# Kernel tuning notes

Hardware: AMD Instinct MI355X
Metric: run time of the kernel (lower is better)

Reference implementation:

```python
import jax, jax.numpy as jnp
import numpy as np

B, S, D, H, SEP = 4, 2048, 768, 8, 102
Dh = D // H


def layer_norm(x, g, b, eps=1e-5):
    m = jnp.mean(x, axis=-1, keepdims=True)
    v = jnp.var(x, axis=-1, keepdims=True)
    return (x - m) / jnp.sqrt(v + eps) * g + b


def setup_inputs() -> dict:
    key = jax.random.key(0)
    ks = jax.random.split(key, 16)
    hidden_states = jax.random.normal(ks[0], (B, S, D), dtype=jnp.float32)
    # input_ids: random vocab ids avoiding SEP, with two SEP tokens planted per row
    rng = np.random.default_rng(0)
    ids = rng.integers(103, 30000, size=(B, S))
    for b in range(B):
        ids[b, S // 3 + 7 * b] = SEP
        ids[b, 2 * S // 3 + 11 * b] = SEP
    input_ids = jnp.asarray(ids, dtype=jnp.int64)
    attention_mask = jnp.ones((B, S), dtype=jnp.int32)
    sc = 0.02
    p = {}
    p['Wq'] = jax.random.normal(ks[1], (D, D), jnp.float32) * sc
    p['bq'] = jnp.zeros((D,), jnp.float32)
    p['Wk'] = jax.random.normal(ks[2], (D, D), jnp.float32) * sc
    p['bk'] = jnp.zeros((D,), jnp.float32)
    p['Wv'] = jax.random.normal(ks[3], (D, D), jnp.float32) * sc
    p['bv'] = jnp.zeros((D,), jnp.float32)
    p['Wo'] = jax.random.normal(ks[4], (D, D), jnp.float32) * sc
    p['bo'] = jnp.zeros((D,), jnp.float32)
    p['ln1_g'] = jnp.ones((D,), jnp.float32)
    p['ln1_b'] = jnp.zeros((D,), jnp.float32)
    p['W1'] = jax.random.normal(ks[5], (D, D), jnp.float32) * sc  # d_ff = d_model
    p['b1'] = jnp.zeros((D,), jnp.float32)
    p['W2'] = jax.random.normal(ks[6], (D, D), jnp.float32) * sc
    p['b2'] = jnp.zeros((D,), jnp.float32)
    p['ln2_g'] = jnp.ones((D,), jnp.float32)
    p['ln2_b'] = jnp.zeros((D,), jnp.float32)
    p['dn_g'] = jnp.ones((D,), jnp.float32)
    p['dn_b'] = jnp.zeros((D,), jnp.float32)
    return dict(hidden_states=hidden_states, input_ids=input_ids,
                attention_mask=attention_mask, **p)


def reference(hidden_states, input_ids, attention_mask,
              Wq, bq, Wk, bk, Wv, bv, Wo, bo, ln1_g, ln1_b,
              W1, b1, W2, b2, ln2_g, ln2_b, dn_g, dn_b):
    x = hidden_states
    # --- SEP-based ragged segment discovery (vectorized over batch) ---
    sep = input_ids == SEP                       # [B,S]
    idx = jnp.arange(S)
    big = S
    first = jnp.min(jnp.where(sep, idx, big), axis=-1)                       # [B]
    second = jnp.min(jnp.where(sep & (idx[None, :] > first[:, None]), idx, big), axis=-1)
    has2 = second < big                          # >= 2 SEP tokens present
    mid = S // 2
    src_end = jnp.where(has2, first, mid)
    hyp_start = jnp.where(has2, first + 1, mid)
    hyp_end = jnp.where(has2, second, S - 1)
    src_mask = (idx[None, :] >= 1) & (idx[None, :] < src_end[:, None])       # keys [B,S]
    hyp_mask = (idx[None, :] >= hyp_start[:, None]) & (idx[None, :] < hyp_end[:, None])
    valid = jnp.any(src_mask, -1) & jnp.any(hyp_mask, -1)                    # [B]

    # --- cross-attention: queries = hyp tokens, keys/values = src tokens ---
    q = (x @ Wq + bq).reshape(B, S, H, Dh)
    k = (x @ Wk + bk).reshape(B, S, H, Dh)
    v = (x @ Wv + bv).reshape(B, S, H, Dh)
    scores = jnp.einsum('bqhd,bkhd->bhqk', q, k) / jnp.sqrt(jnp.float32(Dh))
    scores = jnp.where(src_mask[:, None, None, :], scores, jnp.float32(-1e9))
    attn = jax.nn.softmax(scores, axis=-1)
    ctx = jnp.einsum('bhqk,bkhd->bqhd', attn, v).reshape(B, S, D)
    mha = ctx @ Wo + bo
    x1 = layer_norm(x + mha, ln1_g, ln1_b)
    ffn = jax.nn.gelu(x1 @ W1 + b1) @ W2 + b2
    x2 = layer_norm(x1 + ffn, ln2_g, ln2_b)      # updated_hyp

    # --- diff + LayerNorm, scatter back into hyp segment only ---
    diff = layer_norm(x2 - x, dn_g, dn_b)
    upd = hyp_mask & valid[:, None]
    return jnp.where(upd[..., None], x + diff, x)
```

## Files before the change

### kernel.cpp

```cpp
#include <hip/hip_runtime.h>
#include <math.h>

#define BB 4
#define SS 2048
#define DD 768
#define HH 8
#define DHD 96
#define SEP_ID 102
#define CHUNK 256
#define NCH_MAX 3
#define QT64 11
#define SLOTB 12800

typedef __attribute__((ext_vector_type(8))) short bf16x8;
typedef __attribute__((ext_vector_type(4))) float f32x4;

static __device__ __forceinline__ float gelu_tanh(float x) {
  float x3 = x * x * x;
  float t = tanhf(0.7978845608028654f * (x + 0.044715f * x3));
  return 0.5f * x * (1.0f + t);
}

static __device__ __forceinline__ unsigned short f2bf(float f) {
  unsigned int u = __float_as_uint(f);
  u = (u + 0x7FFF + ((u >> 16) & 1)) >> 16;
  return (unsigned short)u;
}

static __device__ __forceinline__ float bf2f(unsigned short u) {
  return __uint_as_float(((unsigned int)u) << 16);
}

#define MFMA16(A, B, C) __builtin_amdgcn_mfma_f32_16x16x32_bf16(A, B, C, 0, 0, 0)

static __device__ __forceinline__ void gl16(const void* g, void* l) {
  __builtin_amdgcn_global_load_lds(
      (__attribute__((address_space(1))) unsigned int*)g,
      (__attribute__((address_space(3))) unsigned int*)l, 16, 0, 0);
}

__global__ void seg_kernel(const int* __restrict__ ids, int* __restrict__ seg) {
  int b = blockIdx.x;
  const int* row = ids + (size_t)b * SS;
  __shared__ int s1[256], s2[256];
  int m1 = SS, m2 = SS;
  for (int i = threadIdx.x; i < SS; i += 256) {
    if (row[i] == SEP_ID) {
      if (i < m1) { m2 = m1; m1 = i; }
      else if (i < m2) { m2 = i; }
    }
  }
  s1[threadIdx.x] = m1; s2[threadIdx.x] = m2;
  __syncthreads();
  for (int off = 128; off > 0; off >>= 1) {
    if (threadIdx.x < off) {
      int a1 = s1[threadIdx.x], a2 = s2[threadIdx.x];
      int b1 = s1[threadIdx.x + off], b2 = s2[threadIdx.x + off];
      s1[threadIdx.x] = min(a1, b1);
      s2[threadIdx.x] = min(max(a1, b1), min(a2, b2));
    }
    __syncthreads();
  }
  if (threadIdx.x == 0) {
    int first = s1[0], second = s2[0];
    bool has2 = (second < SS);
    int mid = SS / 2;
    int src_end = has2 ? first : mid;
    int hyp_lo = has2 ? (first + 1) : mid;
    int hyp_hi = has2 ? second : (SS - 1);
    int valid = ((src_end - 1) > 0 && (hyp_hi - hyp_lo) > 0) ? 1 : 0;
    if (!valid) { src_end = 1; hyp_lo = 0; hyp_hi = 0; }
    seg[b * 4 + 0] = src_end;
    seg[b * 4 + 1] = hyp_lo;
    seg[b * 4 + 2] = hyp_hi;
    seg[b * 4 + 3] = valid;
  }
}

__global__ void conv_bf(const float* __restrict__ x, unsigned short* __restrict__ xbf, int n4) {
  int i = blockIdx.x * blockDim.x + threadIdx.x;
  int stride = gridDim.x * blockDim.x;
  const float4* xi = (const float4*)x;
  for (; i < n4; i += stride) {
    float4 v = xi[i];
    ushort4 r;
    r.x = f2bf(v.x); r.y = f2bf(v.y); r.z = f2bf(v.z); r.w = f2bf(v.w);
    *(ushort4*)(xbf + (size_t)i * 4) = r;
  }
}

__global__ __launch_bounds__(256) void wtrans6(
    const float* __restrict__ W0, const float* __restrict__ W1,
    const float* __restrict__ W2, const float* __restrict__ W3,
    const float* __restrict__ W4, const float* __restrict__ W5,
    unsigned short* __restrict__ Wt) {
  int z = blockIdx.z;
  const float* W = (z == 0) ? W0 : (z == 1) ? W1 : (z == 2) ? W2
                  : (z == 3) ? W3 : (z == 4) ? W4 : W5;
  unsigned short* O = Wt + (size_t)z * DD * DD;
  __shared__ float t[64][65];
  int k0 = blockIdx.x * 64, n0 = blockIdx.y * 64;
  for (int i = threadIdx.x; i < 4096; i += 256) {
    int kk = i >> 6, nn = i & 63;
    t[kk][nn] = W[(size_t)(k0 + kk) * DD + n0 + nn];
  }
  __syncthreads();
  for (int i = threadIdx.x; i < 4096; i += 256) {
    int nn = i >> 6, kk = i & 63;
    O[(size_t)(n0 + nn) * DD + k0 + kk] = f2bf(t[kk][nn]);
  }
}

__device__ __forceinline__ void gemm_core(
    const unsigned short* __restrict__ A, const unsigned short* __restrict__ Wt,
    const float* __restrict__ bias, unsigned short* __restrict__ C,
    int b, int row0, int hi, int col0, int which, float rs,
    unsigned short (*Al)[64 * 64], unsigned short (*Bl)[128 * 64]) {
  int tid = threadIdx.x, w = tid >> 6, lane = tid & 63;
  int llo = lane & 15, lhi = lane >> 4;
  int wrg = w >> 1, wcg = w & 1;

  const unsigned short* Ab = A + (size_t)b * SS * DD;

  f32x4 acc[2][4];
#pragma unroll
  for (int i = 0; i < 2; ++i)
#pragma unroll
    for (int j = 0; j < 4; ++j) acc[i][j] = (f32x4){0.f, 0.f, 0.f, 0.f};

  auto STAGE = [&](int t, int buf) {
    int kk = t * 64;
#pragma unroll
    for (int j = 0; j < 2; ++j) {
      int s = j * 256 + tid;
      int row = s >> 3, c = s & 7;
      int gr = min(row0 + row, hi - 1);
      gl16(Ab + (size_t)gr * DD + kk + ((c ^ (row & 7)) * 8),
           &Al[buf][(size_t)(j * 256 + w * 64) * 8]);
    }
#pragma unroll
    for (int j = 0; j < 4; ++j) {
      int s = j * 256 + tid;
      int row = s >> 3, c = s & 7;
      gl16(Wt + (size_t)(col0 + row) * DD + kk + ((c ^ (row & 7)) * 8),
           &Bl[buf][(size_t)(j * 256 + w * 64) * 8]);
    }
  };

  STAGE(0, 0);
  __syncthreads();
  for (int t = 0; t < DD / 64; ++t) {
    int cur = t & 1;
    if (t + 1 < DD / 64) STAGE(t + 1, cur ^ 1);
#pragma unroll
    for (int ksub = 0; ksub < 2; ++ksub) {
      bf16x8 af[2], bfr[4];
#pragma unroll
      for (int mi = 0; mi < 2; ++mi) {
        int lr = wrg * 32 + mi * 16 + llo;
        int slot = lr * 8 + ((ksub * 4 + lhi) ^ (lr & 7));
        af[mi] = *(const bf16x8*)&Al[cur][(size_t)slot * 8];
      }
#pragma unroll
      for (int ni = 0; ni < 4; ++ni) {
        int lr = wcg * 64 + ni * 16 + llo;
        int slot = lr * 8 + ((ksub * 4 + lhi) ^ (lr & 7));
        bfr[ni] = *(const bf16x8*)&Bl[cur][(size_t)slot * 8];
      }
#pragma unroll
      for (int mi = 0; mi < 2; ++mi)
#pragma unroll
        for (int ni = 0; ni < 4; ++ni)
          acc[mi][ni] = MFMA16(af[mi], bfr[ni], acc[mi][ni]);
    }
    __syncthreads();
  }

  float osc = (which == 0) ? rs : 1.f;
#pragma unroll
  for (int mi = 0; mi < 2; ++mi)
#pragma unroll
    for (int ni = 0; ni < 4; ++ni) {
      int col = col0 + wcg * 64 + ni * 16 + llo;
      float bsv = bias[col];
      int rowb = row0 + wrg * 32 + mi * 16 + lhi * 4;
#pragma unroll
      for (int r = 0; r < 4; ++r) {
        int row = rowb + r;
        if (row < hi) {
          float v = (acc[mi][ni][r] + bsv) * osc;
          if (which == 4) v = gelu_tanh(v);
          if (which == 2)
            C[((size_t)b * DD + col) * SS + row] = f2bf(v);
          else
            C[((size_t)(b * SS + row)) * DD + col] = f2bf(v);
        }
      }
    }
}

__global__ __launch_bounds__(256) void gemm_qkv(
    const unsigned short* __restrict__ A, const unsigned short* __restrict__ Wt3,
    const float* __restrict__ bq, const float* __restrict__ bk, const float* __restrict__ bv,
    unsigned short* __restrict__ Qo, unsigned short* __restrict__ Ko,
    unsigned short* __restrict__ Vto, const int* __restrict__ seg, float rs) {
  __shared__ unsigned short Al[2][64 * 64];
  __shared__ unsigned short Bl[2][128 * 64];
  int b = blockIdx.z;
  int which = blockIdx.x / 6;
  int col0 = (blockIdx.x % 6) * 128;
  int lo = (which == 0) ? seg[b * 4 + 1] : 1;
  int hi = (which == 0) ? seg[b * 4 + 2] : seg[b * 4 + 0];
  int row0 = lo + (int)blockIdx.y * 64;
  if (row0 >= hi) return;
  const unsigned short* Wt = Wt3 + (size_t)which * DD * DD;
  const float* bias = (which == 0) ? bq : (which == 1) ? bk : bv;
  unsigned short* C = (which == 0) ? Qo : (which == 1) ? Ko : Vto;
  gemm_core(A, Wt, bias, C, b, row0, hi, col0, which, rs, Al, Bl);
}

__global__ __launch_bounds__(256) void gemm_mfma(
    const unsigned short* __restrict__ A, const unsigned short* __restrict__ Wt,
    const float* __restrict__ bias, unsigned short* __restrict__ C,
    const int* __restrict__ seg, int gelu) {
  __shared__ unsigned short Al[2][64 * 64];
  __shared__ unsigned short Bl[2][128 * 64];
  int b = blockIdx.z;
  int lo = seg[b * 4 + 1], hi = seg[b * 4 + 2];
  int row0 = lo + (int)blockIdx.y * 64;
  if (row0 >= hi) return;
  gemm_core(A, Wt, bias, C, b, row0, hi, (int)blockIdx.x * 128,
            gelu ? 4 : 3, 1.f, Al, Bl);
}

__global__ __launch_bounds__(256) void attn_split(
    const unsigned short* __restrict__ Q, const unsigned short* __restrict__ K,
    const unsigned short* __restrict__ Vt, char* __restrict__ part,
    const int* __restrict__ seg) {
  int bh = blockIdx.z;
  int b = bh >> 3, h = bh & 7;
  int src_hi = seg[b * 4 + 0];
  int hyp_lo = seg[b * 4 + 1], hyp_hi = seg[b * 4 + 2];
  int q0b = hyp_lo + (int)blockIdx.x * 64;
  if (q0b >= hyp_hi) return;
  int ks = 1 + (int)blockIdx.y * CHUNK;
  if (ks >= src_hi) return;
  int ke = min(ks + CHUNK, src_hi);

  __shared__ unsigned short kls[64 * 128];
  __shared__ unsigned short vls[96 * 64];
  __shared__ unsigned short plds[4][1024];

  int tid = threadIdx.x;
  int w = tid >> 6, lane = tid & 63;
  int llo = lane & 15, lhi = lane >> 4;

  int qrow = min(q0b + w * 16 + llo, hyp_hi - 1);
  const unsigned short* qbase = Q + ((size_t)(b * SS + qrow)) * DD + h * DHD;
  bf16x8 qf[3];
#pragma unroll
  for (int df = 0; df < 3; ++df)
    qf[df] = *(const bf16x8*)(qbase + df * 32 + lhi * 8);

  const unsigned short* Kb = K + (size_t)b * SS * DD + h * DHD;
  const unsigned short* Vb = Vt + ((size_t)b * DD + h * DHD) * SS;

  f32x4 acc[6];
#pragma unroll
  for (int dt = 0; dt < 6; ++dt) acc[dt] = (f32x4){0.f, 0.f, 0.f, 0.f};
  float m_r[4] = {-1e30f, -1e30f, -1e30f, -1e30f};
  float l_r[4] = {0.f, 0.f, 0.f, 0.f};

  for (int k0 = ks; k0 < ke; k0 += 64) {
    __syncthreads();
#pragma unroll
    for (int p = 0; p < 3; ++p) {
      int idx = tid + p * 256;
      int row = idx / 12, slot = idx - row * 12;
      int krow = min(k0 + row, ke - 1);
      bf16x8 v = *(const bf16x8*)(Kb + (size_t)krow * DD + slot * 8);
      *(bf16x8*)&kls[row * 128 + ((slot ^ (row & 7)) << 3)] = v;
    }
#pragma unroll
    for (int p = 0; p < 3; ++p) {
      int idx = tid + p * 256;
      int row = idx >> 3, slot = idx & 7;
      bf16x8 v = *(const bf16x8*)(Vb + (size_t)row * SS + k0 + slot * 8);
      *(bf16x8*)&vls[row * 64 + ((slot ^ (row & 7)) << 3)] = v;
    }
    __syncthreads();
    f32x4 s[4];
#pragma unroll
    for (int t = 0; t < 4; ++t) {
      f32x4 st = (f32x4){0.f, 0.f, 0.f, 0.f};
      int row = t * 16 + llo;
#pragma unroll
      for (int df = 0; df < 3; ++df) {
        int slot = df * 4 + lhi;
        bf16x8 kf = *(const bf16x8*)&kls[row * 128 + ((slot ^ (row & 7)) << 3)];
        st = MFMA16(qf[df], kf, st);
      }
      s[t] = st;
    }
    float mx[4] = {-1e30f, -1e30f, -1e30f, -1e30f};
#pragma unroll
    for (int t = 0; t < 4; ++t) {
      bool kv = (k0 + t * 16 + llo) < ke;
#pragma unroll
      for (int r = 0; r < 4; ++r) {
        float sv = kv ? s[t][r] : -1e30f;
        s[t][r] = sv;
        mx[r] = fmaxf(mx[r], sv);
      }
    }
#pragma unroll
    for (int st = 1; st < 16; st <<= 1)
#pragma unroll
      for (int r = 0; r < 4; ++r) mx[r] = fmaxf(mx[r], __shfl_xor(mx[r], st));

    float p[4][4];
#pragma unroll
    for (int r = 0; r < 4; ++r) {
      float mn = fmaxf(m_r[r], mx[r]);
      float sc = __expf(m_r[r] - mn);
      m_r[r] = mn;
      l_r[r] *= sc;
#pragma unroll
      for (int dt = 0; dt < 6; ++dt) acc[dt][r] *= sc;
      float ps = 0.f;
#pragma unroll
      for (int t = 0; t < 4; ++t) {
        float pv = (s[t][r] > -1e29f) ? __expf(s[t][r] - mn) : 0.f;
        p[t][r] = pv;
        ps += pv;
      }
#pragma unroll
      for (int st = 1; st < 16; st <<= 1) ps += __shfl_xor(ps, st);
      l_r[r] += ps;
    }
#pragma unroll
    for (int t = 0; t < 4; ++t)
#pragma unroll
      for (int r = 0; r < 4; ++r) {
        int qq = lhi * 4 + r, kk = t * 16 + llo;
        plds[w][qq * 64 + (kk ^ ((qq & 7) << 3))] = f2bf(p[t][r]);
      }
    bf16x8 pa[2];
#pragma unroll
    for (int kh = 0; kh < 2; ++kh) {
      int idx = llo * 64 + ((lhi * 8 + kh * 32) ^ ((llo & 7) << 3));
      pa[kh] = *(const bf16x8*)&plds[w][idx];
    }
#pragma unroll
    for (int dt = 0; dt < 6; ++dt) {
      int row = dt * 16 + llo;
#pragma unroll
      for (int kh = 0; kh < 2; ++kh) {
        int slot = kh * 4 + lhi;
        bf16x8 vf = *(const bf16x8*)&vls[row * 64 + ((slot ^ (row & 7)) << 3)];
        acc[dt] = MFMA16(pa[kh], vf, acc[dt]);
      }
    }
  }
  char* slot = part + (((size_t)bh * QT64 + blockIdx.x) * NCH_MAX + blockIdx.y) * SLOTB;
  unsigned short* pacc = (unsigned short*)slot;
  float* pml = (float*)(slot + 12288);
#pragma unroll
  for (int r = 0; r < 4; ++r) {
    int qq = w * 16 + lhi * 4 + r;
#pragma unroll
    for (int dt = 0; dt < 6; ++dt)
      pacc[qq * 96 + dt * 16 + llo] = f2bf(acc[dt][r]);
    if (llo == 0) { pml[qq] = m_r[r]; pml[64 + qq] = l_r[r]; }
  }
}

__global__ __launch_bounds__(128) void attn_reduce(
    const char* __restrict__ part, unsigned short* __restrict__ ctx,
    const int* __restrict__ seg) {
  int bh = blockIdx.y;
  int b = bh >> 3, h = bh & 7;
  int src_hi = seg[b * 4 + 0];
  int hyp_lo = seg[b * 4 + 1], hyp_hi = seg[b * 4 + 2];
  int q0 = hyp_lo + (int)blockIdx.x * 16;
  if (q0 >= hyp_hi) return;
  int nch = (src_hi - 1 + CHUNK - 1) / CHUNK;
  if (nch > NCH_MAX) nch = NCH_MAX;
  int sub = blockIdx.x & 3;

  __shared__ float ml[NCH_MAX][32];
  __shared__ float Mg[16], invL[16], sc[NCH_MAX][16];
  int tid = threadIdx.x;
  const char* base = part + ((size_t)bh * QT64 + (blockIdx.x >> 2)) * NCH_MAX * SLOTB;
  for (int i = tid; i < 32 * nch; i += 128) {
    int c = i >> 5, j = i & 31;
    const float* pml = (const float*)(base + c * SLOTB + 12288);
    ml[c][j] = (j < 16) ? pml[sub * 16 + j] : pml[64 + sub * 16 + (j - 16)];
  }
  __syncthreads();
  if (tid < 16) {
    float mg = -1e30f;
    for (int c = 0; c < nch; ++c) mg = fmaxf(mg, ml[c][tid]);
    float lg = 0.f;
    for (int c = 0; c < nch; ++c) lg += ml[c][16 + tid] * __expf(ml[c][tid] - mg);
    Mg[tid] = mg;
    invL[tid] = 1.f / lg;
  }
  __syncthreads();
  for (int i = tid; i < 16 * nch; i += 128) {
    int c = i >> 4, q = i & 15;
    sc[c][q] = __expf(ml[c][q] - Mg[q]);
  }
  __syncthreads();
  for (int i = tid; i < 1536; i += 128) {
    int q = i / 96, d = i - q * 96;
    float v = 0.f;
    for (int c = 0; c < nch; ++c)
      v += bf2f(((const unsigned short*)(base + c * SLOTB))[(sub * 16 + q) * 96 + d]) * sc[c][q];
    int qq = q0 + q;
    if (qq < hyp_hi)
      ctx[((size_t)(b * SS + qq)) * DD + h * DHD + d] = f2bf(v * invL[q]);
  }
}

__device__ __forceinline__ float block_sum(float v, float* sbuf) {
#pragma unroll
  for (int off = 32; off > 0; off >>= 1) v += __shfl_xor(v, off);
  int lane = threadIdx.x & 63, w = threadIdx.x >> 6;
  __syncthreads();
  if (lane == 0) sbuf[w] = v;
  __syncthreads();
  return sbuf[0] + sbuf[1] + sbuf[2] + sbuf[3];
}

__global__ __launch_bounds__(256) void ln_residual(
    const float* __restrict__ X, const unsigned short* __restrict__ Yin,
    const float* __restrict__ g, const float* __restrict__ bta,
    float* __restrict__ Out, unsigned short* __restrict__ OutBf,
    const int* __restrict__ seg) {
  int b = blockIdx.y;
  int row = seg[b * 4 + 1] + (int)blockIdx.x;
  if (row >= seg[b * 4 + 2]) return;
  __shared__ float sbuf[4];
  size_t base = ((size_t)(b * SS + row)) * DD;
  int tid = threadIdx.x;
  float v[3];
  float sum = 0.f;
#pragma unroll
  for (int r = 0; r < 3; ++r) {
    int i = tid + r * 256;
    v[r] = X[base + i] + bf2f(Yin[base + i]);
    sum += v[r];
  }
  float mean = block_sum(sum, sbuf) * (1.f / DD);
  float vs = 0.f;
#pragma unroll
  for (int r = 0; r < 3; ++r) { float d = v[r] - mean; vs += d * d; }
  float var = block_sum(vs, sbuf) * (1.f / DD);
  float inv = rsqrtf(var + 1e-5f);
#pragma unroll
  for (int r = 0; r < 3; ++r) {
    int i = tid + r * 256;
    float o = (v[r] - mean) * inv * g[i] + bta[i];
    Out[base + i] = o;
    OutBf[base + i] = f2bf(o);
  }
}

__global__ __launch_bounds__(256) void ln2_diff_scatter(
    const float* __restrict__ X, const float* __restrict__ X1,
    const unsigned short* __restrict__ T2,
    const float* __restrict__ g2, const float* __restrict__ b2,
    const float* __restrict__ gd, const float* __restrict__ bd,
    float* __restrict__ Out, const int* __restrict__ seg) {
  int b = blockIdx.y, row = blockIdx.x;
  size_t base = ((size_t)(b * SS + row)) * DD;
  int tid = threadIdx.x;
  if (row < seg[b * 4 + 1] || row >= seg[b * 4 + 2]) {
#pragma unroll
    for (int r = 0; r < 3; ++r) {
      int i = tid + r * 256;
      Out[base + i] = X[base + i];
    }
    return;
  }
  __shared__ float sbuf[4];
  float y[3], xv[3];
  float sum = 0.f;
#pragma unroll
  for (int r = 0; r < 3; ++r) {
    int i = tid + r * 256;
    y[r] = X1[base + i] + bf2f(T2[base + i]);
    xv[r] = X[base + i];
    sum += y[r];
  }
  float mean = block_sum(sum, sbuf) * (1.f / DD);
  float vs = 0.f;
#pragma unroll
  for (int r = 0; r < 3; ++r) { float d = y[r] - mean; vs += d * d; }
  float var = block_sum(vs, sbuf) * (1.f / DD);
  float inv = rsqrtf(var + 1e-5f);
  float z[3];
  float sum2 = 0.f;
#pragma unroll
  for (int r = 0; r < 3; ++r) {
    int i = tid + r * 256;
    float x2 = (y[r] - mean) * inv * g2[i] + b2[i];
    z[r] = x2 - xv[r];
    sum2 += z[r];
  }
  float mean2 = block_sum(sum2, sbuf) * (1.f / DD);
  float vs2 = 0.f;
#pragma unroll
  for (int r = 0; r < 3; ++r) { float d = z[r] - mean2; vs2 += d * d; }
  float var2 = block_sum(vs2, sbuf) * (1.f / DD);
  float inv2 = rsqrtf(var2 + 1e-5f);
#pragma unroll
  for (int r = 0; r < 3; ++r) {
    int i = tid + r * 256;
    Out[base + i] = xv[r] + (z[r] - mean2) * inv2 * gd[i] + bd[i];
  }
}

extern "C" void kernel_launch(void* const* d_in, const int* in_sizes, int n_in,
                              void* d_out, int out_size, void* d_ws, size_t ws_size,
                              hipStream_t stream) {
  const float* x = (const float*)d_in[0];
  const int* ids = (const int*)d_in[1];
  const float* Wq = (const float*)d_in[3];
  const float* bq = (const float*)d_in[4];
  const float* Wk = (const float*)d_in[5];
  const float* bk = (const float*)d_in[6];
  const float* Wv = (const float*)d_in[7];
  const float* bv = (const float*)d_in[8];
  const float* Wo = (const float*)d_in[9];
  const float* bo = (const float*)d_in[10];
  const float* ln1g = (const float*)d_in[11];
  const float* ln1b = (const float*)d_in[12];
  const float* W1 = (const float*)d_in[13];
  const float* b1 = (const float*)d_in[14];
  const float* W2 = (const float*)d_in[15];
  const float* b2 = (const float*)d_in[16];
  const float* ln2g = (const float*)d_in[17];
  const float* ln2b = (const float*)d_in[18];
  const float* dng = (const float*)d_in[19];
  const float* dnb = (const float*)d_in[20];
  float* out = (float*)d_out;

  char* ws = (char*)d_ws;
  int* seg = (int*)ws;
  size_t NBH = (size_t)BB * SS * DD * 2;
  char* Ap = ws + 256;
  char* Bp = Ap + NBH;
  char* Cp = Bp + NBH;
  char* Dp = Cp + NBH;
  char* Fp = Dp + NBH + 8192;
  char* Gp = Fp + (size_t)BB * SS * DD * 4;

  unsigned short* x_bf = (unsigned short*)Ap;
  unsigned short* ctx_bf = (unsigned short*)Ap;
  unsigned short* h1_bf = (unsigned short*)Ap;
  unsigned short* q_bf = (unsigned short*)Bp;
  unsigned short* mha_bf = (unsigned short*)Bp;
  unsigned short* k_bf = (unsigned short*)Cp;
  unsigned short* t2_bf = (unsigned short*)Cp;
  unsigned short* vt_bf = (unsigned short*)Dp;
  unsigned short* x1_bf = (unsigned short*)Dp;
  char* part = Fp;
  float* x1f = (float*)Fp;
  unsigned short* wt = (unsigned short*)Gp;
  const size_t WSZ = (size_t)DD * DD;

  const float rs = 0.1020620726159658f;

  seg_kernel<<<BB, 256, 0, stream>>>(ids, seg);
  conv_bf<<<1536, 256, 0, stream>>>(x, x_bf, BB * SS * DD / 4);
  wtrans6<<<dim3(DD / 64, DD / 64, 6), 256, 0, stream>>>(Wq, Wk, Wv, Wo, W1, W2, wt);
  hipMemsetAsync(Dp, 0, NBH + 8192, stream);

  gemm_qkv<<<dim3(18, 11, BB), 256, 0, stream>>>(
      x_bf, wt, bq, bk, bv, q_bf, k_bf, vt_bf, seg, rs);

  attn_split<<<dim3(QT64, NCH_MAX, 32), 256, 0, stream>>>(q_bf, k_bf, vt_bf, part, seg);
  attn_reduce<<<dim3(44, 32), 128, 0, stream>>>(part, ctx_bf, seg);

  gemm_mfma<<<dim3(6, 11, BB), 256, 0, stream>>>(ctx_bf, wt + 3 * WSZ, bo, mha_bf, seg, 0);
  ln_residual<<<dim3(704, BB), 256, 0, stream>>>(x, mha_bf, ln1g, ln1b, x1f, x1_bf, seg);
  gemm_mfma<<<dim3(6, 11, BB), 256, 0, stream>>>(x1_bf, wt + 4 * WSZ, b1, h1_bf, seg, 1);
  gemm_mfma<<<dim3(6, 11, BB), 256, 0, stream>>>(h1_bf, wt + 5 * WSZ, b2, t2_bf, seg, 0);
  ln2_diff_scatter<<<dim3(SS, BB), 256, 0, stream>>>(x, x1f, t2_bf, ln2g, ln2b, dng, dnb, out, seg);
}
```

Before: 175.6 us.

## Fuse prep kernels into one launch and drop memset via V zero-padding

Merges segment discovery, the bf16 conversion of x and the weight transposes into a single block-indexed prep kernel, cutting three launches to one. Removes the hipMemsetAsync of the V-transpose buffer: the QKV GEMM now writes zeros for padded rows past the source end and launches one extra row tile so the padding is covered. This saves launch and memset overhead, but the correctness of the padding depends on attention reading only up to hi+64 rows and on nothing else relying on the zeroed region.

```diff
diff --git a/kernel.cpp b/kernel.cpp
--- a/kernel.cpp
+++ b/kernel.cpp
@@ -39,75 +39,79 @@
       (__attribute__((address_space(3))) unsigned int*)l, 16, 0, 0);
 }
 
-__global__ void seg_kernel(const int* __restrict__ ids, int* __restrict__ seg) {
-  int b = blockIdx.x;
-  const int* row = ids + (size_t)b * SS;
-  __shared__ int s1[256], s2[256];
-  int m1 = SS, m2 = SS;
-  for (int i = threadIdx.x; i < SS; i += 256) {
-    if (row[i] == SEP_ID) {
-      if (i < m1) { m2 = m1; m1 = i; }
-      else if (i < m2) { m2 = i; }
-    }
-  }
-  s1[threadIdx.x] = m1; s2[threadIdx.x] = m2;
-  __syncthreads();
-  for (int off = 128; off > 0; off >>= 1) {
-    if (threadIdx.x < off) {
-      int a1 = s1[threadIdx.x], a2 = s2[threadIdx.x];
-      int b1 = s1[threadIdx.x + off], b2 = s2[threadIdx.x + off];
-      s1[threadIdx.x] = min(a1, b1);
-      s2[threadIdx.x] = min(max(a1, b1), min(a2, b2));
-    }
-    __syncthreads();
-  }
-  if (threadIdx.x == 0) {
-    int first = s1[0], second = s2[0];
-    bool has2 = (second < SS);
-    int mid = SS / 2;
-    int src_end = has2 ? first : mid;
-    int hyp_lo = has2 ? (first + 1) : mid;
-    int hyp_hi = has2 ? second : (SS - 1);
-    int valid = ((src_end - 1) > 0 && (hyp_hi - hyp_lo) > 0) ? 1 : 0;
-    if (!valid) { src_end = 1; hyp_lo = 0; hyp_hi = 0; }
-    seg[b * 4 + 0] = src_end;
-    seg[b * 4 + 1] = hyp_lo;
-    seg[b * 4 + 2] = hyp_hi;
-    seg[b * 4 + 3] = valid;
-  }
-}
-
-__global__ void conv_bf(const float* __restrict__ x, unsigned short* __restrict__ xbf, int n4) {
-  int i = blockIdx.x * blockDim.x + threadIdx.x;
-  int stride = gridDim.x * blockDim.x;
-  const float4* xi = (const float4*)x;
-  for (; i < n4; i += stride) {
-    float4 v = xi[i];
-    ushort4 r;
-    r.x = f2bf(v.x); r.y = f2bf(v.y); r.z = f2bf(v.z); r.w = f2bf(v.w);
-    *(ushort4*)(xbf + (size_t)i * 4) = r;
-  }
-}
-
-__global__ __launch_bounds__(256) void wtrans6(
+__global__ __launch_bounds__(256) void prep(
+    const int* __restrict__ ids, int* __restrict__ seg,
+    const float* __restrict__ x, unsigned short* __restrict__ xbf, int n4,
     const float* __restrict__ W0, const float* __restrict__ W1,
     const float* __restrict__ W2, const float* __restrict__ W3,
     const float* __restrict__ W4, const float* __restrict__ W5,
     unsigned short* __restrict__ Wt) {
-  int z = blockIdx.z;
-  const float* W = (z == 0) ? W0 : (z == 1) ? W1 : (z == 2) ? W2
-                  : (z == 3) ? W3 : (z == 4) ? W4 : W5;
-  unsigned short* O = Wt + (size_t)z * DD * DD;
-  __shared__ float t[64][65];
-  int k0 = blockIdx.x * 64, n0 = blockIdx.y * 64;
-  for (int i = threadIdx.x; i < 4096; i += 256) {
-    int kk = i >> 6, nn = i & 63;
-    t[kk][nn] = W[(size_t)(k0 + kk) * DD + n0 + nn];
-  }
-  __syncthreads();
-  for (int i = threadIdx.x; i < 4096; i += 256) {
-    int nn = i >> 6, kk = i & 63;
-    O[(size_t)(n0 + nn) * DD + k0 + kk] = f2bf(t[kk][nn]);
+  __shared__ char smem[64 * 65 * 4];
+  int bx = blockIdx.x;
+  if (bx < 4) {
+    int* s1 = (int*)smem;
+    int* s2 = s1 + 256;
+    int b = bx;
+    const int* row = ids + (size_t)b * SS;
+    int m1 = SS, m2 = SS;
+    for (int i = threadIdx.x; i < SS; i += 256) {
+      if (row[i] == SEP_ID) {
+        if (i < m1) { m2 = m1; m1 = i; }
+        else if (i < m2) { m2 = i; }
+      }
+    }
+    s1[threadIdx.x] = m1; s2[threadIdx.x] = m2;
+    __syncthreads();
+    for (int off = 128; off > 0; off >>= 1) {
+      if (threadIdx.x < off) {
+        int a1 = s1[threadIdx.x], a2 = s2[threadIdx.x];
+        int b1 = s1[threadIdx.x + off], b2 = s2[threadIdx.x + off];
+        s1[threadIdx.x] = min(a1, b1);
+        s2[threadIdx.x] = min(max(a1, b1), min(a2, b2));
+      }
+      __syncthreads();
+    }
+    if (threadIdx.x == 0) {
+      int first = s1[0], second = s2[0];
+      bool has2 = (second < SS);
+      int mid = SS / 2;
+      int src_end = has2 ? first : mid;
+      int hyp_lo = has2 ? (first + 1) : mid;
+      int hyp_hi = has2 ? second : (SS - 1);
+      int valid = ((src_end - 1) > 0 && (hyp_hi - hyp_lo) > 0) ? 1 : 0;
+      if (!valid) { src_end = 1; hyp_lo = 0; hyp_hi = 0; }
+      seg[b * 4 + 0] = src_end;
+      seg[b * 4 + 1] = hyp_lo;
+      seg[b * 4 + 2] = hyp_hi;
+      seg[b * 4 + 3] = valid;
+    }
+  } else if (bx < 1540) {
+    int i = (bx - 4) * 256 + threadIdx.x;
+    int stride = 1536 * 256;
+    const float4* xi = (const float4*)x;
+    for (; i < n4; i += stride) {
+      float4 v = xi[i];
+      ushort4 r;
+      r.x = f2bf(v.x); r.y = f2bf(v.y); r.z = f2bf(v.z); r.w = f2bf(v.w);
+      *(ushort4*)(xbf + (size_t)i * 4) = r;
+    }
+  } else {
+    float (*t)[65] = (float(*)[65])smem;
+    int idx = bx - 1540;
+    int z = idx / 144, rem = idx - z * 144;
+    const float* W = (z == 0) ? W0 : (z == 1) ? W1 : (z == 2) ? W2
+                    : (z == 3) ? W3 : (z == 4) ? W4 : W5;
+    unsigned short* O = Wt + (size_t)z * DD * DD;
+    int k0 = (rem / 12) * 64, n0 = (rem % 12) * 64;
+    for (int i = threadIdx.x; i < 4096; i += 256) {
+      int kk = i >> 6, nn = i & 63;
+      t[kk][nn] = W[(size_t)(k0 + kk) * DD + n0 + nn];
+    }
+    __syncthreads();
+    for (int i = threadIdx.x; i < 4096; i += 256) {
+      int nn = i >> 6, kk = i & 63;
+      O[(size_t)(n0 + nn) * DD + k0 + kk] = f2bf(t[kk][nn]);
+    }
   }
 }
 
@@ -187,13 +191,14 @@
 #pragma unroll
       for (int r = 0; r < 4; ++r) {
         int row = rowb + r;
-        if (row < hi) {
+        if (which == 2) {
+          float v = acc[mi][ni][r] + bsv;
+          C[((size_t)b * DD + col) * SS + row] =
+              (row < hi) ? f2bf(v) : (unsigned short)0;
+        } else if (row < hi) {
           float v = (acc[mi][ni][r] + bsv) * osc;
           if (which == 4) v = gelu_tanh(v);
-          if (which == 2)
-            C[((size_t)b * DD + col) * SS + row] = f2bf(v);
-          else
-            C[((size_t)(b * SS + row)) * DD + col] = f2bf(v);
+          C[((size_t)(b * SS + row)) * DD + col] = f2bf(v);
         }
       }
     }
@@ -212,7 +217,7 @@
   int lo = (which == 0) ? seg[b * 4 + 1] : 1;
   int hi = (which == 0) ? seg[b * 4 + 2] : seg[b * 4 + 0];
   int row0 = lo + (int)blockIdx.y * 64;
-  if (row0 >= hi) return;
+  if (row0 >= hi && !(which == 2 && row0 < hi + 64)) return;
   const unsigned short* Wt = Wt3 + (size_t)which * DD * DD;
   const float* bias = (which == 0) ? bq : (which == 1) ? bk : bv;
   unsigned short* C = (which == 0) ? Qo : (which == 1) ? Ko : Vto;
@@ -573,12 +578,10 @@
 
   const float rs = 0.1020620726159658f;
 
-  seg_kernel<<<BB, 256, 0, stream>>>(ids, seg);
-  conv_bf<<<1536, 256, 0, stream>>>(x, x_bf, BB * SS * DD / 4);
-  wtrans6<<<dim3(DD / 64, DD / 64, 6), 256, 0, stream>>>(Wq, Wk, Wv, Wo, W1, W2, wt);
-  hipMemsetAsync(Dp, 0, NBH + 8192, stream);
-
-  gemm_qkv<<<dim3(18, 11, BB), 256, 0, stream>>>(
+  prep<<<2404, 256, 0, stream>>>(ids, seg, x, x_bf, BB * SS * DD / 4,
+                                 Wq, Wk, Wv, Wo, W1, W2, wt);
+
+  gemm_qkv<<<dim3(18, 12, BB), 256, 0, stream>>>(
       x_bf, wt, bq, bk, bv, q_bf, k_bf, vt_bf, seg, rs);
 
   attn_split<<<dim3(QT64, NCH_MAX, 32), 256, 0, stream>>>(q_bf, k_bf, vt_bf, part, seg);
```

New measurement: 166.3 us. -5.3%, faster.
